# Optimization experiments

Hardware: AMD Instinct MI355X
Metric: run time of the kernel (lower is better)

## Reference

```python
import jax, jax.numpy as jnp
import numpy as np

C = 256
DEPTH = 4
GRIDS = [(128, 128), (128, 128), (128, 128)]
B = 2
N = 32768


def _ln_c(x, g, b):
    # LayerNorm over channel dim of [B, C, N] (myLayerNorm transposes to [B,N,C])
    m = x.mean(axis=1, keepdims=True)
    v = ((x - m) ** 2).mean(axis=1, keepdims=True)
    return (x - m) * jax.lax.rsqrt(v + 1e-5) * g[None, :, None] + b[None, :, None]


def _bn_train(x, g, b):
    # BatchNorm1d (training-mode batch stats) over [B, C, L]
    m = x.mean(axis=(0, 2), keepdims=True)
    v = ((x - m) ** 2).mean(axis=(0, 2), keepdims=True)
    return (x - m) * jax.lax.rsqrt(v + 1e-5) * g[None, :, None] + b[None, :, None]


def _dwconv3(x, w, b):
    # depthwise 3x3 conv, SAME padding; x [B,C,H,W], w [C,3,3]
    out = jax.lax.conv_general_dilated(x, w[:, None, :, :], (1, 1), 'SAME',
                                       feature_group_count=C,
                                       dimension_numbers=('NCHW', 'OIHW', 'NCHW'))
    return out + b[None, :, None, None]


def setup_inputs() -> dict:
    key = jax.random.key(0)
    ks = jax.random.split(key, 20)
    tokens = jax.random.normal(ks[0], (B, C, N), jnp.float32)
    hw = GRIDS[0][0] * GRIDS[0][1]
    cell_ind = jax.random.randint(ks[1], (B, 3, N), 0, hw)
    occupied_cell = jnp.ones((B, N), jnp.float32)

    def p(k, shape, scale=0.05):
        return scale * jax.random.normal(k, shape, jnp.float32)

    inp = dict(tokens=tokens, cell_ind=cell_ind, occupied_cell=occupied_cell)
    inp['smix_ln_g'] = 1.0 + p(ks[2], (DEPTH, C))
    inp['smix_ln_b'] = p(ks[3], (DEPTH, C))
    inp['ffn_w1'] = p(ks[4], (DEPTH, C, 3, 3), 0.2)
    inp['ffn_b1'] = p(ks[5], (DEPTH, C))
    inp['ffn_w2'] = p(ks[6], (DEPTH, C, 3, 3), 0.2)
    inp['ffn_b2'] = p(ks[7], (DEPTH, C))
    inp['att_scale'] = 1.0 + p(ks[8], (DEPTH, C))
    inp['att_bn_g'] = 1.0 + p(ks[9], (DEPTH, C))
    inp['att_bn_b'] = p(ks[10], (DEPTH, C))
    inp['cmix_ln_g'] = 1.0 + p(ks[11], (DEPTH, C))
    inp['cmix_ln_b'] = p(ks[12], (DEPTH, C))
    inp['cmix_w1'] = p(ks[13], (DEPTH, C, C), 1.0 / float(np.sqrt(C)))
    inp['cmix_b1'] = p(ks[14], (DEPTH, C))
    inp['cmix_w2'] = p(ks[15], (DEPTH, C, C), 1.0 / float(np.sqrt(C)))
    inp['cmix_b2'] = p(ks[16], (DEPTH, C))
    inp['cmix_scale'] = p(ks[17], (DEPTH, C), 0.1)
    return inp


def _forward(tokens, occupied_cell, cell_ind,
             smix_ln_g, smix_ln_b, ffn_w1, ffn_b1, ffn_w2, ffn_b2,
             att_scale, att_bn_g, att_bn_b,
             cmix_ln_g, cmix_ln_b, cmix_w1, cmix_b1, cmix_w2, cmix_b2, cmix_scale):
    Bx, Cx, Nx = tokens.shape
    bidx = jnp.arange(Bx)[:, None]
    # build_proj_matrix equivalent: per-point 1/(points-in-cell) weights + clamped indices
    sp = []
    for g in range(len(GRIDS)):
        HW = GRIDS[g][0] * GRIDS[g][1]
        ci = jnp.clip(cell_ind[:, g], 0, HW - 1)
        # inflate^T @ occupied: per-cell occupied count (occupied^2 per point)
        counts = jnp.zeros((Bx, HW), tokens.dtype).at[bidx, ci].add(occupied_cell * occupied_cell)
        # inflate @ counts: per-point count of points sharing its cell
        npp = occupied_cell * jnp.take_along_axis(counts, ci, axis=1)
        sp.append((ci, occupied_cell / (npp + 1e-6)))
    skip = [jnp.zeros(GRIDS[g], tokens.dtype) for g in range(len(GRIDS))]
    for d in range(DEPTH):
        g = d % len(GRIDS)
        H, W = GRIDS[g]
        HW = H * W
        ci, wpt = sp[g]
        # --- SpatialMix ---
        r = _ln_c(tokens, smix_ln_g[d], smix_ln_b[d]) * wpt[:, None, :]
        grid = jnp.zeros((Bx, Cx, HW), tokens.dtype).at[
            jnp.arange(Bx)[:, None, None], jnp.arange(Cx)[None, :, None], ci[:, None, :]].add(r)
        grid = grid.reshape(Bx, Cx, H, W) + skip[g]
        plane = _dwconv3(jax.nn.relu(_dwconv3(grid, ffn_w1[d], ffn_b1[d])), ffn_w2[d], ffn_b2[d])
        rflat = plane.reshape(Bx, Cx, HW)
        att = jax.nn.sigmoid(_bn_train(rflat * att_scale[d][None, :, None], att_bn_g[d], att_bn_b[d]))
        rflat = att * rflat
        r = jnp.take_along_axis(rflat, jnp.broadcast_to(ci[:, None, :], (Bx, Cx, Nx)), axis=2)
        tokens = tokens + r
        skip[g] = plane
        # --- ChannelMix ---
        h = _ln_c(tokens, cmix_ln_g[d], cmix_ln_b[d])
        h = jnp.einsum('oc,bcn->bon', cmix_w1[d], h) + cmix_b1[d][None, :, None]
        h = jnp.einsum('oc,bcn->bon', cmix_w2[d], jax.nn.relu(h)) + cmix_b2[d][None, :, None]
        tokens = tokens + h * cmix_scale[d][None, :, None]
    return tokens


def reference(tokens, cell_ind, occupied_cell,
              smix_ln_g, smix_ln_b, ffn_w1, ffn_b1, ffn_w2, ffn_b2,
              att_scale, att_bn_g, att_bn_b,
              cmix_ln_g, cmix_ln_b, cmix_w1, cmix_b1, cmix_w2, cmix_b2, cmix_scale):
    return _forward(tokens, occupied_cell, cell_ind,
                    smix_ln_g, smix_ln_b, ffn_w1, ffn_b1, ffn_w2, ffn_b2,
                    att_scale, att_bn_g, att_bn_b,
                    cmix_ln_g, cmix_ln_b, cmix_w1, cmix_b1, cmix_w2, cmix_b2, cmix_scale)
```

## Files before the change

### kernel.cpp

```cpp
#include <hip/hip_runtime.h>
#include <hip/hip_bf16.h>
#include <hip/hip_fp16.h>

#define Cc 256
#define Nn 32768
#define HWc 16384
#define Bb 2

typedef float floatx4 __attribute__((ext_vector_type(4)));
typedef short bf16x8 __attribute__((ext_vector_type(8)));
typedef unsigned short ushort8v __attribute__((ext_vector_type(8)));
typedef unsigned short ushort4v __attribute__((ext_vector_type(4)));

__device__ __forceinline__ unsigned short f2b(float f){
    unsigned u = __float_as_uint(f);
    u += 0x7fff + ((u >> 16) & 1);
    return (unsigned short)(u >> 16);
}
__device__ __forceinline__ float b2f(unsigned short h){
    return __uint_as_float(((unsigned)h) << 16);
}
__device__ __forceinline__ unsigned short f2h(float f){
    return __half_as_ushort(__float2half(f));
}
__device__ __forceinline__ float h2f(unsigned short h){
    return __half2float(__ushort_as_half(h));
}

__global__ __launch_bounds__(256) void k_count(const int* __restrict__ ci,
                                               const float* __restrict__ occ,
                                               float* __restrict__ fcounts,
                                               int* __restrict__ icounts){
    int idx = blockIdx.x*256 + threadIdx.x;
    if (idx >= Bb*3*Nn) return;
    int n = idx & (Nn-1);
    int bg = idx >> 15;
    int b = bg / 3;
    int cell = min(max(ci[idx], 0), HWc-1);
    float o = occ[(b<<15) + n];
    atomicAdd(&fcounts[(bg<<14) + cell], o*o);
    atomicAdd(&icounts[(bg<<14) + cell], 1);
}

__global__ __launch_bounds__(256) void k_wpt(const int* __restrict__ ci,
                                             const float* __restrict__ occ,
                                             const float* __restrict__ fcounts,
                                             float* __restrict__ wpt){
    int idx = blockIdx.x*256 + threadIdx.x;
    if (idx >= Bb*3*Nn) return;
    int n = idx & (Nn-1);
    int bg = idx >> 15;
    int b = bg / 3;
    int cell = min(max(ci[idx], 0), HWc-1);
    float o = occ[(b<<15) + n];
    float cnt = fcounts[(bg<<14) + cell];
    wpt[idx] = o / (o*cnt + 1e-6f);
}

__global__ __launch_bounds__(256) void k_scan(const int* __restrict__ ic,
                                              int* __restrict__ starts,
                                              int* __restrict__ cursor){
    __shared__ int part[256];
    int bg = blockIdx.x;
    int t = threadIdx.x;
    const int* cs = ic + (bg << 14);
    int base = t * 64;
    int s = 0;
    for (int i = 0; i < 64; ++i) s += cs[base + i];
    part[t] = s;
    __syncthreads();
    for (int off = 1; off < 256; off <<= 1){
        int v = (t >= off) ? part[t - off] : 0;
        __syncthreads();
        part[t] += v;
        __syncthreads();
    }
    int run = (t == 0) ? 0 : part[t - 1];
    int* st = starts + bg * (HWc + 1);
    int* cu = cursor + (bg << 14);
    for (int i = 0; i < 64; ++i){
        st[base + i] = run;
        cu[base + i] = run;
        run += cs[base + i];
    }
    if (t == 255) st[HWc] = run;
}

__global__ __launch_bounds__(256) void k_fill(const int* __restrict__ ci,
                                              int* __restrict__ cursor,
                                              int* __restrict__ plist){
    int idx = blockIdx.x*256 + threadIdx.x;
    if (idx >= Bb*3*Nn) return;
    int n = idx & (Nn-1);
    int bg = idx >> 15;
    int cell = min(max(ci[idx], 0), HWc-1);
    int pos = atomicAdd(&cursor[(bg<<14) + cell], 1);
    plist[(bg<<15) + pos] = n;
}

__global__ __launch_bounds__(256) void k_wcvt(const float* __restrict__ w1,
                                              const float* __restrict__ w2,
                                              unsigned short* __restrict__ W1b,
                                              unsigned short* __restrict__ W2b){
    int idx = blockIdx.x*256 + threadIdx.x;
    if (idx >= 4*Cc*Cc) return;
    W1b[idx] = f2b(w1[idx]);
    W2b[idx] = f2b(w2[idx]);
}

__global__ __launch_bounds__(512, 4) void k1a_ln(const float* __restrict__ tok,
                                              const float* __restrict__ wpt,
                                              const float* __restrict__ lng,
                                              const float* __restrict__ lnb,
                                              unsigned short* __restrict__ rbuf, int g){
    __shared__ float reds[512], redq[512];
    __shared__ float m_s[64], r_s[64];
    __shared__ float lg[Cc], lb[Cc];
    int tid = threadIdx.x;
    int bi = blockIdx.x;
    int b = bi >> 9;
    int p0 = (bi & 511) << 6;
    if (tid < 256){ lg[tid] = lng[tid]; lb[tid] = lnb[tid]; }
    int p  = tid & 63;
    int cg = tid >> 6;
    int c0 = cg << 5;
    const float* tb = tok + ((size_t)b << 8)*Nn + p0 + p;
    float vreg[32];
    float sum = 0.f, sq = 0.f;
    #pragma unroll
    for (int k = 0; k < 32; ++k){
        float v = tb[(size_t)(c0 + k) << 15];
        vreg[k] = v; sum += v; sq += v*v;
    }
    reds[tid] = sum; redq[tid] = sq;
    __syncthreads();
    if (tid < 64){
        float s = 0.f, q = 0.f;
        #pragma unroll
        for (int j = 0; j < 8; ++j){ s += reds[j*64 + tid]; q += redq[j*64 + tid]; }
        float m = s * (1.f/256.f);
        float var = q * (1.f/256.f) - m*m;
        m_s[tid] = m;
        r_s[tid] = rsqrtf(fmaxf(var, 0.f) + 1e-5f);
    }
    __syncthreads();
    float mp = m_s[p], rp = r_s[p];
    float wv = wpt[(b*3 + g)*Nn + p0 + p];
    unsigned short* rb = rbuf + ((size_t)((b << 15) + p0 + p))*Cc + c0;
    #pragma unroll
    for (int j = 0; j < 4; ++j){
        ushort8v u;
        #pragma unroll
        for (int e = 0; e < 8; ++e){
            int k = j*8 + e, c = c0 + k;
            u[e] = f2h(((vreg[k] - mp)*rp*lg[c] + lb[c]) * wv);
        }
        *(ushort8v*)(rb + 8*j) = u;
    }
}

__global__ __launch_bounds__(256) void k1b_gather(const unsigned short* __restrict__ rbuf,
                                                  const int* __restrict__ starts,
                                                  const int* __restrict__ plist,
                                                  unsigned short* __restrict__ grid,
                                                  float* __restrict__ bnSQ, int g){
    int t = threadIdx.x;
    int bi = blockIdx.x;
    if (bi == 0){ bnSQ[t] = 0.f; bnSQ[256 + t] = 0.f; }
    int b = bi >> 11;
    int cell0 = (bi & 2047) << 3;
    int bg = b*3 + g;
    const int* st = starts + bg*(HWc + 1) + cell0;
    const int* pl = plist + (bg << 15);
    const unsigned short* rb = rbuf + (((size_t)b << 15) << 8);
    float acc[8];
    int s0 = st[0];
    #pragma unroll
    for (int q = 0; q < 8; ++q){
        int s1 = st[q + 1];
        float a = 0.f;
        for (int j = s0; j < s1; ++j){
            int p = pl[j];
            a += h2f(rb[((size_t)p << 8) + t]);
        }
        acc[q] = a;
        s0 = s1;
    }
    unsigned short* go = grid + ((size_t)((b << 8) + t))*HWc + cell0;
    ushort8v u;
    #pragma unroll
    for (int e = 0; e < 8; ++e) u[e] = f2h(acc[e]);
    *(ushort8v*)go = u;
}

__global__ __launch_bounds__(256) void k2_conv(const unsigned short* __restrict__ grid,
                                               const unsigned short* __restrict__ skip,
                                               unsigned short* __restrict__ plane,
                                               const float* __restrict__ w1, const float* __restrict__ b1,
                                               const float* __restrict__ w2, const float* __restrict__ b2,
                                               const float* __restrict__ asc,
                                               float* __restrict__ bnS, float* __restrict__ bnQ,
                                               int useskip){
    __shared__ float it[36*136];
    __shared__ float mid[34*136];
    int tid = threadIdx.x;
    int bi = blockIdx.x;
    int rt = bi & 3;
    int bc = bi >> 2;
    int c = bc & 255;
    int r0 = rt << 5;
    const unsigned short* src = grid + (size_t)bc*HWc;
    const unsigned short* sk  = skip + (size_t)bc*HWc;
    for (int i = tid; i < 36; i += 256){
        it[i*136 + 0] = 0.f;   it[i*136 + 1] = 0.f;
        it[i*136 + 130] = 0.f; it[i*136 + 131] = 0.f;
        it[i*136 + 132] = 0.f; it[i*136 + 133] = 0.f;
    }
    for (int i = tid; i < 36*16; i += 256){
        int r = i >> 4, ch = i & 15;
        int gy = r0 - 2 + r;
        float vals[8];
        #pragma unroll
        for (int e = 0; e < 8; ++e) vals[e] = 0.f;
        if ((unsigned)gy < 128u){
            ushort8v sv = *(const ushort8v*)(src + (gy << 7) + ch*8);
            if (useskip){
                ushort8v kv = *(const ushort8v*)(sk + (gy << 7) + ch*8);
                #pragma unroll
                for (int e = 0; e < 8; ++e) vals[e] = h2f(sv[e]) + h2f(kv[e]);
            } else {
                #pragma unroll
                for (int e = 0; e < 8; ++e) vals[e] = h2f(sv[e]);
            }
        }
        #pragma unroll
        for (int e = 0; e < 8; ++e) it[r*136 + 2 + ch*8 + e] = vals[e];
    }
    float a1[9], a2[9];
    #pragma unroll
    for (int j = 0; j < 9; ++j){ a1[j] = w1[c*9+j]; a2[j] = w2[c*9+j]; }
    float bb1 = b1[c], bb2 = b2[c], sc = asc[c];
    __syncthreads();
    for (int i = tid; i < 34*33; i += 256){
        int r = i / 33, chk = i - r*33;
        int cc0 = chk << 2;
        int y = r0 - 1 + r;
        bool yok = (unsigned)y < 128u;
        float o0 = 0.f, o1 = 0.f, o2 = 0.f, o3 = 0.f;
        if (yok){
            #pragma unroll
            for (int jr = 0; jr < 3; ++jr){
                const float* row = &it[(r + jr)*136 + cc0];
                floatx4 a = *(const floatx4*)row;
                float a4 = row[4], a5 = row[5];
                float w0 = a1[jr*3+0], w1v = a1[jr*3+1], w2v = a1[jr*3+2];
                o0 += w0*a[0] + w1v*a[1] + w2v*a[2];
                o1 += w0*a[1] + w1v*a[2] + w2v*a[3];
                o2 += w0*a[2] + w1v*a[3] + w2v*a4;
                o3 += w0*a[3] + w1v*a4  + w2v*a5;
            }
        }
        float* mrow = &mid[r*136 + cc0];
        mrow[0] = (yok && cc0+0 >= 1 && cc0+0 <= 128) ? fmaxf(o0 + bb1, 0.f) : 0.f;
        mrow[1] = (yok && cc0+1 >= 1 && cc0+1 <= 128) ? fmaxf(o1 + bb1, 0.f) : 0.f;
        mrow[2] = (yok && cc0+2 >= 1 && cc0+2 <= 128) ? fmaxf(o2 + bb1, 0.f) : 0.f;
        mrow[3] = (yok && cc0+3 >= 1 && cc0+3 <= 128) ? fmaxf(o3 + bb1, 0.f) : 0.f;
    }
    __syncthreads();
    float ps = 0.f, pq = 0.f;
    unsigned short* dst = plane + (size_t)bc*HWc;
    for (int i = tid; i < 32*32; i += 256){
        int yy = i >> 5, chk = i & 31;
        int x0 = chk << 2;
        float o0 = 0.f, o1 = 0.f, o2 = 0.f, o3 = 0.f;
        #pragma unroll
        for (int jr = 0; jr < 3; ++jr){
            const float* row = &mid[(yy + jr)*136 + x0];
            floatx4 a = *(const floatx4*)row;
            float a4 = row[4], a5 = row[5];
            float w0 = a2[jr*3+0], w1v = a2[jr*3+1], w2v = a2[jr*3+2];
            o0 += w0*a[0] + w1v*a[1] + w2v*a[2];
            o1 += w0*a[1] + w1v*a[2] + w2v*a[3];
            o2 += w0*a[2] + w1v*a[3] + w2v*a4;
            o3 += w0*a[3] + w1v*a4  + w2v*a5;
        }
        float v0 = o0 + bb2, v1 = o1 + bb2, v2 = o2 + bb2, v3 = o3 + bb2;
        ushort4v u;
        u[0] = f2h(v0); u[1] = f2h(v1); u[2] = f2h(v2); u[3] = f2h(v3);
        *(ushort4v*)(dst + ((r0 + yy) << 7) + x0) = u;
        float t0 = v0*sc, t1 = v1*sc, t2 = v2*sc, t3 = v3*sc;
        ps += t0 + t1 + t2 + t3;
        pq += t0*t0 + t1*t1 + t2*t2 + t3*t3;
    }
    __syncthreads();
    it[tid] = ps; it[256 + tid] = pq;
    __syncthreads();
    for (int s2 = 128; s2 > 0; s2 >>= 1){
        if (tid < s2){ it[tid] += it[tid+s2]; it[256+tid] += it[256+tid+s2]; }
        __syncthreads();
    }
    if (tid == 0){
        atomicAdd(&bnS[c], it[0]);
        atomicAdd(&bnQ[c], it[256]);
    }
}

__global__ __launch_bounds__(256) void k3t_att_t(const unsigned short* __restrict__ plane,
                                                 const float* __restrict__ bnS, const float* __restrict__ bnQ,
                                                 const float* __restrict__ asc,
                                                 const float* __restrict__ bng, const float* __restrict__ bnb,
                                                 unsigned short* __restrict__ attp){
    __shared__ float t[32*33];
    __shared__ float P_s[32], Q_s[32];
    int tid = threadIdx.x;
    int tx = tid & 31, ty = tid >> 5;
    int bi = blockIdx.x;
    int ht = bi & 511;
    int ct = (bi >> 9) & 7;
    int b  = bi >> 12;
    int c0 = ct << 5, h0 = ht << 5;
    if (tid < 32){
        int c = c0 + tid;
        float mean = bnS[c] * (1.f/32768.f);
        float var  = bnQ[c] * (1.f/32768.f) - mean*mean;
        float inv  = rsqrtf(fmaxf(var, 0.f) + 1e-5f) * bng[c];
        P_s[tid] = asc[c] * inv;
        Q_s[tid] = bnb[c] - mean * inv;
    }
    __syncthreads();
    for (int r = ty; r < 32; r += 8){
        int c = c0 + r;
        float v = h2f(plane[(((size_t)b << 8) + c)*HWc + h0 + tx]);
        float s = 1.f / (1.f + __expf(-(P_s[r]*v + Q_s[r])));
        t[r*33 + tx] = s * v;
    }
    __syncthreads();
    for (int r = ty; r < 32; r += 8){
        attp[(((size_t)b << 14) + h0 + r)*Cc + c0 + tx] = f2h(t[tx*33 + r]);
    }
}

__global__ __launch_bounds__(512, 4) void k4_cmix(const float* __restrict__ tsrc, int tin_nc,
                                               float* __restrict__ tdst, int tout_nc,
                                               const unsigned short* __restrict__ attp,
                                               const int* __restrict__ ci,
                                               const unsigned short* __restrict__ W1,
                                               const unsigned short* __restrict__ W2,
                                               const float* __restrict__ lng, const float* __restrict__ lnb,
                                               const float* __restrict__ b1, const float* __restrict__ b2,
                                               const float* __restrict__ csc,
                                               const float* __restrict__ lng2, const float* __restrict__ lnb2,
                                               const float* __restrict__ wptb,
                                               unsigned short* __restrict__ rbufn,
                                               int g, int g2, int donext){
    __shared__ __align__(16) unsigned short hs[64*264];
    __shared__ float reds[512], redq[512];
    __shared__ float m_s[64], r_s[64];
    __shared__ int cell_s[64];
    __shared__ float lng_s[Cc], lnb_s[Cc], b1_s[Cc], b2s_s[Cc], cs_s[Cc], g2g_s[Cc], g2b_s[Cc];

    int tid = threadIdx.x;
    int bi = blockIdx.x;
    int b = bi >> 9;
    int p0 = (bi & 511) << 6;

    if (tid < 256){
        lng_s[tid] = lng[tid];
        lnb_s[tid] = lnb[tid];
        b1_s[tid]  = b1[tid];
        float cv = csc[tid];
        cs_s[tid]  = cv;
        b2s_s[tid] = b2[tid] * cv;
        g2g_s[tid] = lng2[tid];
        g2b_s[tid] = lnb2[tid];
    }
    if (tid < 64){
        int cc = ci[(b*3 + g)*Nn + p0 + tid];
        cell_s[tid] = min(max(cc, 0), HWc-1);
    }
    __syncthreads();

    int p  = tid & 63;
    int cg = tid >> 6;
    int c0 = cg << 5;

    const unsigned short* ar = attp + ((size_t)((b << 14) + cell_s[p]))*Cc + c0;
    ushort8v rr[4];
    #pragma unroll
    for (int j = 0; j < 4; ++j) rr[j] = *(const ushort8v*)(ar + 8*j);

    float vreg[32];
    float sum = 0.f, sq = 0.f;
    if (tin_nc){
        const floatx4* tn4 = (const floatx4*)(tsrc + ((((size_t)(b << 15)) + p0 + p) << 8) + c0);
        #pragma unroll
        for (int j = 0; j < 8; ++j){
            floatx4 f = tn4[j];
            #pragma unroll
            for (int e = 0; e < 4; ++e){
                int k = j*4 + e;
                float v = f[e] + h2f(rr[k >> 3][k & 7]);
                vreg[k] = v; sum += v; sq += v*v;
            }
        }
    } else {
        const float* tb = tsrc + ((size_t)b << 8)*Nn + p0 + p;
        #pragma unroll
        for (int k = 0; k < 32; ++k){
            float v = tb[(size_t)(c0 + k) << 15] + h2f(rr[k >> 3][k & 7]);
            vreg[k] = v; sum += v; sq += v*v;
        }
    }
    reds[tid] = sum; redq[tid] = sq;
    __syncthreads();
    if (tid < 64){
        float s = 0.f, q = 0.f;
        #pragma unroll
        for (int j = 0; j < 8; ++j){ s += reds[j*64 + tid]; q += redq[j*64 + tid]; }
        float m = s * (1.f/256.f);
        float var = q * (1.f/256.f) - m*m;
        m_s[tid] = m;
        r_s[tid] = rsqrtf(fmaxf(var, 0.f) + 1e-5f);
    }
    __syncthreads();
    float mp = m_s[p], rp = r_s[p];
    unsigned short* hrow = &hs[p*264 + c0];
    #pragma unroll
    for (int j = 0; j < 4; ++j){
        ushort8v u;
        #pragma unroll
        for (int e = 0; e < 8; ++e){
            int k = j*8 + e, c = c0 + k;
            u[e] = f2b((vreg[k] - mp)*rp*lng_s[c] + lnb_s[c]);
        }
        *(ushort8v*)(hrow + 8*j) = u;
    }
    __syncthreads();

    int lane = tid & 63;
    int w = tid >> 6;
    int l15 = lane & 15;
    int q4 = lane >> 4;
    floatx4 acc[2][4];
    #pragma unroll
    for (int mi = 0; mi < 2; ++mi)
        #pragma unroll
        for (int ni = 0; ni < 4; ++ni)
            acc[mi][ni] = (floatx4){0.f, 0.f, 0.f, 0.f};

    #pragma unroll
    for (int kk = 0; kk < 8; ++kk){
        int k0 = kk*32 + q4*8;
        bf16x8 bfr[4];
        #pragma unroll
        for (int ni = 0; ni < 4; ++ni)
            bfr[ni] = *(const bf16x8*)&hs[(ni*16 + l15)*264 + k0];
        #pragma unroll
        for (int mi = 0; mi < 2; ++mi){
            bf16x8 af = *(const bf16x8*)&W1[(size_t)(w*32 + mi*16 + l15)*Cc + k0];
            #pragma unroll
            for (int ni = 0; ni < 4; ++ni)
                acc[mi][ni] = __builtin_amdgcn_mfma_f32_16x16x32_bf16(af, bfr[ni], acc[mi][ni], 0, 0, 0);
        }
    }
    __syncthreads();
    #pragma unroll
    for (int mi = 0; mi < 2; ++mi)
        #pragma unroll
        for (int ni = 0; ni < 4; ++ni){
            int m0 = w*32 + mi*16 + q4*4;
            int nn = ni*16 + l15;
            ushort4v u;
            #pragma unroll
            for (int r = 0; r < 4; ++r)
                u[r] = f2b(fmaxf(acc[mi][ni][r] + b1_s[m0 + r], 0.f));
            *(ushort4v*)&hs[nn*264 + m0] = u;
        }
    __syncthreads();

    #pragma unroll
    for (int mi = 0; mi < 2; ++mi)
        #pragma unroll
        for (int ni = 0; ni < 4; ++ni)
            acc[mi][ni] = (floatx4){0.f, 0.f, 0.f, 0.f};
    #pragma unroll
    for (int kk = 0; kk < 8; ++kk){
        int k0 = kk*32 + q4*8;
        bf16x8 bfr[4];
        #pragma unroll
        for (int ni = 0; ni < 4; ++ni)
            bfr[ni] = *(const bf16x8*)&hs[(ni*16 + l15)*264 + k0];
        #pragma unroll
        for (int mi = 0; mi < 2; ++mi){
            bf16x8 af = *(const bf16x8*)&W2[(size_t)(w*32 + mi*16 + l15)*Cc + k0];
            #pragma unroll
            for (int ni = 0; ni < 4; ++ni)
                acc[mi][ni] = __builtin_amdgcn_mfma_f32_16x16x32_bf16(af, bfr[ni], acc[mi][ni], 0, 0, 0);
        }
    }
    __syncthreads();
    #pragma unroll
    for (int mi = 0; mi < 2; ++mi)
        #pragma unroll
        for (int ni = 0; ni < 4; ++ni){
            int m0 = w*32 + mi*16 + q4*4;
            int nn = ni*16 + l15;
            ushort4v u;
            #pragma unroll
            for (int r = 0; r < 4; ++r)
                u[r] = f2b(acc[mi][ni][r]*cs_s[m0 + r] + b2s_s[m0 + r]);
            *(ushort4v*)&hs[nn*264 + m0] = u;
        }
    __syncthreads();

    float sum2 = 0.f, sq2 = 0.f;
    if (tout_nc){
        float* tn = tdst + ((((size_t)(b << 15)) + p0 + p) << 8) + c0;
        #pragma unroll
        for (int j = 0; j < 4; ++j){
            ushort8v u = *(const ushort8v*)(hrow + 8*j);
            floatx4 fa, fb;
            #pragma unroll
            for (int e = 0; e < 4; ++e){
                int k = j*8 + e;
                float v = vreg[k] + b2f(u[e]);
                vreg[k] = v; fa[e] = v; sum2 += v; sq2 += v*v;
            }
            #pragma unroll
            for (int e = 4; e < 8; ++e){
                int k = j*8 + e;
                float v = vreg[k] + b2f(u[e]);
                vreg[k] = v; fb[e-4] = v; sum2 += v; sq2 += v*v;
            }
            *(floatx4*)(tn + 8*j) = fa;
            *(floatx4*)(tn + 8*j + 4) = fb;
        }
    } else {
        float* ob = tdst + ((size_t)b << 8)*Nn + p0 + p;
        #pragma unroll
        for (int j = 0; j < 4; ++j){
            ushort8v u = *(const ushort8v*)(hrow + 8*j);
            #pragma unroll
            for (int e = 0; e < 8; ++e){
                int k = j*8 + e, c = c0 + k;
                float v = vreg[k] + b2f(u[e]);
                vreg[k] = v;
                ob[(size_t)c << 15] = v;
                sum2 += v; sq2 += v*v;
            }
        }
    }
    if (donext){
        reds[tid] = sum2; redq[tid] = sq2;
        __syncthreads();
        if (tid < 64){
            float s = 0.f, q = 0.f;
            #pragma unroll
            for (int j = 0; j < 8; ++j){ s += reds[j*64 + tid]; q += redq[j*64 + tid]; }
            float m = s * (1.f/256.f);
            float var = q * (1.f/256.f) - m*m;
            m_s[tid] = m;
            r_s[tid] = rsqrtf(fmaxf(var, 0.f) + 1e-5f);
        }
        __syncthreads();
        float m2 = m_s[p], rr2 = r_s[p];
        float wv2 = wptb[(b*3 + g2)*Nn + p0 + p];
        unsigned short* rb = rbufn + ((size_t)((b << 15) + p0 + p))*Cc + c0;
        #pragma unroll
        for (int j = 0; j < 4; ++j){
            ushort8v u;
            #pragma unroll
            for (int e = 0; e < 8; ++e){
                int k = j*8 + e, c = c0 + k;
                u[e] = f2h(((vreg[k] - m2)*rr2*g2g_s[c] + g2b_s[c]) * wv2);
            }
            *(ushort8v*)(rb + 8*j) = u;
        }
    }
}

extern "C" void kernel_launch(void* const* d_in, const int* in_sizes, int n_in,
                              void* d_out, int out_size, void* d_ws, size_t ws_size,
                              hipStream_t stream){
    (void)in_sizes; (void)n_in; (void)out_size;
    const float* tokens  = (const float*)d_in[0];
    const int*   cellind = (const int*)d_in[1];
    const float* occ     = (const float*)d_in[2];
    const float* smix_g  = (const float*)d_in[3];
    const float* smix_b  = (const float*)d_in[4];
    const float* ffn_w1  = (const float*)d_in[5];
    const float* ffn_b1  = (const float*)d_in[6];
    const float* ffn_w2  = (const float*)d_in[7];
    const float* ffn_b2  = (const float*)d_in[8];
    const float* att_sc  = (const float*)d_in[9];
    const float* bn_g    = (const float*)d_in[10];
    const float* bn_b    = (const float*)d_in[11];
    const float* cm_g    = (const float*)d_in[12];
    const float* cm_b    = (const float*)d_in[13];
    const float* cw1     = (const float*)d_in[14];
    const float* cb1     = (const float*)d_in[15];
    const float* cw2     = (const float*)d_in[16];
    const float* cb2     = (const float*)d_in[17];
    const float* cscale  = (const float*)d_in[18];
    float* out = (float*)d_out;
    char* w = (char*)d_ws;

    const size_t HGRID_BYTES = (size_t)Bb*Cc*HWc*2;
    unsigned short* grid_h  = (unsigned short*)(w);
    unsigned short* attp_h  = grid_h;
    unsigned short* planeA  = (unsigned short*)(w + HGRID_BYTES);
    unsigned short* planeB  = (unsigned short*)(w + 2*HGRID_BYTES);
    unsigned short* rbuf    = (unsigned short*)(w + 3*HGRID_BYTES);
    size_t o = 3*HGRID_BYTES + (size_t)Bb*Nn*Cc*2;
    float* fcounts = (float*)(w + o); o += (size_t)Bb*3*HWc*4;
    int*   icounts = (int*)(w + o);   o += (size_t)Bb*3*HWc*4;
    float* wptb   = (float*)(w + o); o += (size_t)Bb*3*Nn*4;
    float* bnS    = (float*)(w + o);
    float* bnQ    = bnS + 256;
    o += 4096;
    unsigned short* W1b = (unsigned short*)(w + o);
    unsigned short* W2b = W1b + 4*Cc*Cc;
    o += (size_t)2*4*Cc*Cc*2;
    int* startsb  = (int*)(w + o); o += (size_t)Bb*3*(HWc+1)*4;
    int* cursors  = (int*)(w + o); o += (size_t)Bb*3*HWc*4;
    int* plistb   = (int*)(w + o); o += (size_t)Bb*3*Nn*4;
    o = (o + 255) & ~(size_t)255;
    float* tnc    = (float*)(w + o);
    size_t needed = o + (size_t)Bb*Nn*Cc*4;
    int nc_ok = (ws_size >= needed) ? 1 : 0;

    hipMemsetAsync(fcounts, 0, (size_t)2*Bb*3*HWc*4, stream);
    k_count<<<(Bb*3*Nn)/256, 256, 0, stream>>>(cellind, occ, fcounts, icounts);
    k_wpt<<<(Bb*3*Nn)/256, 256, 0, stream>>>(cellind, occ, fcounts, wptb);
    k_scan<<<Bb*3, 256, 0, stream>>>(icounts, startsb, cursors);
    k_fill<<<(Bb*3*Nn)/256, 256, 0, stream>>>(cellind, cursors, plistb);
    k_wcvt<<<(4*Cc*Cc)/256, 256, 0, stream>>>(cw1, cw2, W1b, W2b);

    k1a_ln<<<Bb*(Nn/64), 512, 0, stream>>>(tokens, wptb, smix_g, smix_b, rbuf, 0);

    for (int d = 0; d < 4; ++d){
        int g = d % 3;
        int g2 = (d + 1) % 3;
        int donext = (d < 3) ? 1 : 0;
        int useskip = (d == 3) ? 1 : 0;
        unsigned short* plane = (d == 0) ? planeA : planeB;
        int dn = (d + 1 < 4) ? d + 1 : d;

        const float* tsrc; int tin_nc;
        float* tdst; int tout_nc;
        if (nc_ok){
            tsrc = (d == 0) ? tokens : tnc;  tin_nc  = (d == 0) ? 0 : 1;
            tdst = (d == 3) ? out : tnc;     tout_nc = (d == 3) ? 0 : 1;
        } else {
            tsrc = (d == 0) ? tokens : out;  tin_nc  = 0;
            tdst = out;                      tout_nc = 0;
        }

        k1b_gather<<<Bb*(HWc/8), 256, 0, stream>>>(rbuf, startsb, plistb, grid_h, bnS, g);
        k2_conv<<<Bb*Cc*4, 256, 0, stream>>>(grid_h, planeA, plane,
                                             ffn_w1 + d*Cc*9, ffn_b1 + d*Cc,
                                             ffn_w2 + d*Cc*9, ffn_b2 + d*Cc,
                                             att_sc + d*Cc, bnS, bnQ, useskip);
        k3t_att_t<<<Bb*8*512, 256, 0, stream>>>(plane, bnS, bnQ, att_sc + d*Cc,
                                                bn_g + d*Cc, bn_b + d*Cc, attp_h);
        k4_cmix<<<Bb*(Nn/64), 512, 0, stream>>>(tsrc, tin_nc, tdst, tout_nc, attp_h, cellind,
                                                W1b + (size_t)d*Cc*Cc, W2b + (size_t)d*Cc*Cc,
                                                cm_g + d*Cc, cm_b + d*Cc,
                                                cb1 + d*Cc, cb2 + d*Cc, cscale + d*Cc,
                                                smix_g + dn*Cc, smix_b + dn*Cc, wptb,
                                                rbuf, g, g2, donext);
    }
}
```

Baseline: 702.9 us.

## Add specialized token-major channel-mix kernel for middle depths and fuse setup kernels

Adds k4_cmix_nc, a version of the channel-mix kernel for depths 1-2 that reads and writes tokens in [B,N,C] layout. It keeps the hidden activations in LDS, runs both 256x256 projections with bf16 MFMA, and produces the next layer's normalized, weighted rbuf in one pass. The setup path folds the weight-per-token kernel into the fill kernel, vectorizes the scan with int4 loads and stores, and pads the starts stride to keep those accesses aligned. The aim is fewer launches and less generic indexing on the middle layers, at the cost of a second code path to keep correct.

```diff
diff --git a/kernel.cpp b/kernel.cpp
--- a/kernel.cpp
+++ b/kernel.cpp
@@ -6,11 +6,13 @@
 #define Nn 32768
 #define HWc 16384
 #define Bb 2
+#define STS (HWc + 16)
 
 typedef float floatx4 __attribute__((ext_vector_type(4)));
 typedef short bf16x8 __attribute__((ext_vector_type(8)));
 typedef unsigned short ushort8v __attribute__((ext_vector_type(8)));
 typedef unsigned short ushort4v __attribute__((ext_vector_type(4)));
+typedef int int4v __attribute__((ext_vector_type(4)));
 
 __device__ __forceinline__ unsigned short f2b(float f){
     unsigned u = __float_as_uint(f);
@@ -42,10 +44,48 @@
     atomicAdd(&icounts[(bg<<14) + cell], 1);
 }
 
-__global__ __launch_bounds__(256) void k_wpt(const int* __restrict__ ci,
-                                             const float* __restrict__ occ,
-                                             const float* __restrict__ fcounts,
-                                             float* __restrict__ wpt){
+__global__ __launch_bounds__(256) void k_scan(const int* __restrict__ ic,
+                                              int* __restrict__ starts,
+                                              int* __restrict__ cursor){
+    __shared__ int part[256];
+    int bg = blockIdx.x;
+    int t = threadIdx.x;
+    const int* cs = ic + (bg << 14);
+    int4v buf[16];
+    int s = 0;
+    #pragma unroll
+    for (int i = 0; i < 16; ++i){
+        buf[i] = *(const int4v*)(cs + t*64 + i*4);
+        s += buf[i][0] + buf[i][1] + buf[i][2] + buf[i][3];
+    }
+    part[t] = s;
+    __syncthreads();
+    for (int off = 1; off < 256; off <<= 1){
+        int v = (t >= off) ? part[t - off] : 0;
+        __syncthreads();
+        part[t] += v;
+        __syncthreads();
+    }
+    int run = (t == 0) ? 0 : part[t - 1];
+    int* st = starts + bg * STS;
+    int* cu = cursor + (bg << 14);
+    #pragma unroll
+    for (int i = 0; i < 16; ++i){
+        int4v o;
+        #pragma unroll
+        for (int e = 0; e < 4; ++e){ o[e] = run; run += buf[i][e]; }
+        *(int4v*)(st + t*64 + i*4) = o;
+        *(int4v*)(cu + t*64 + i*4) = o;
+    }
+    if (t == 255) st[HWc] = run;
+}
+
+__global__ __launch_bounds__(256) void k_fill(const int* __restrict__ ci,
+                                              const float* __restrict__ occ,
+                                              const float* __restrict__ fcounts,
+                                              int* __restrict__ cursor,
+                                              int* __restrict__ plist,
+                                              float* __restrict__ wpt){
     int idx = blockIdx.x*256 + threadIdx.x;
     if (idx >= Bb*3*Nn) return;
     int n = idx & (Nn-1);
@@ -55,45 +95,6 @@
     float o = occ[(b<<15) + n];
     float cnt = fcounts[(bg<<14) + cell];
     wpt[idx] = o / (o*cnt + 1e-6f);
-}
-
-__global__ __launch_bounds__(256) void k_scan(const int* __restrict__ ic,
-                                              int* __restrict__ starts,
-                                              int* __restrict__ cursor){
-    __shared__ int part[256];
-    int bg = blockIdx.x;
-    int t = threadIdx.x;
-    const int* cs = ic + (bg << 14);
-    int base = t * 64;
-    int s = 0;
-    for (int i = 0; i < 64; ++i) s += cs[base + i];
-    part[t] = s;
-    __syncthreads();
-    for (int off = 1; off < 256; off <<= 1){
-        int v = (t >= off) ? part[t - off] : 0;
-        __syncthreads();
-        part[t] += v;
-        __syncthreads();
-    }
-    int run = (t == 0) ? 0 : part[t - 1];
-    int* st = starts + bg * (HWc + 1);
-    int* cu = cursor + (bg << 14);
-    for (int i = 0; i < 64; ++i){
-        st[base + i] = run;
-        cu[base + i] = run;
-        run += cs[base + i];
-    }
-    if (t == 255) st[HWc] = run;
-}
-
-__global__ __launch_bounds__(256) void k_fill(const int* __restrict__ ci,
-                                              int* __restrict__ cursor,
-                                              int* __restrict__ plist){
-    int idx = blockIdx.x*256 + threadIdx.x;
-    if (idx >= Bb*3*Nn) return;
-    int n = idx & (Nn-1);
-    int bg = idx >> 15;
-    int cell = min(max(ci[idx], 0), HWc-1);
     int pos = atomicAdd(&cursor[(bg<<14) + cell], 1);
     plist[(bg<<15) + pos] = n;
 }
@@ -170,7 +171,7 @@
     int b = bi >> 11;
     int cell0 = (bi & 2047) << 3;
     int bg = b*3 + g;
-    const int* st = starts + bg*(HWc + 1) + cell0;
+    const int* st = starts + bg*STS + cell0;
     const int* pl = plist + (bg << 15);
     const unsigned short* rb = rbuf + (((size_t)b << 15) << 8);
     float acc[8];
@@ -576,6 +577,184 @@
             }
             *(ushort8v*)(rb + 8*j) = u;
         }
+    }
+}
+
+__global__ __launch_bounds__(512, 4) void k4_cmix_nc(const float* __restrict__ tsrc,
+                                               float* __restrict__ tdst,
+                                               const unsigned short* __restrict__ attp,
+                                               const int* __restrict__ ci,
+                                               const unsigned short* __restrict__ W1,
+                                               const unsigned short* __restrict__ W2,
+                                               const float* __restrict__ lng, const float* __restrict__ lnb,
+                                               const float* __restrict__ b1, const float* __restrict__ b2,
+                                               const float* __restrict__ csc,
+                                               const float* __restrict__ lng2, const float* __restrict__ lnb2,
+                                               const float* __restrict__ wptb,
+                                               unsigned short* __restrict__ rbufn,
+                                               int g, int g2){
+    __shared__ __align__(16) unsigned short hs[64*264];
+    __shared__ float b1_s[Cc], b2s_s[Cc], cs_s[Cc];
+
+    int tid = threadIdx.x;
+    int lane = tid & 63;
+    int w = tid >> 6;
+    int bi = blockIdx.x;
+    int b = bi >> 9;
+    int p0 = (bi & 511) << 6;
+    int c4 = lane << 2;
+
+    if (tid < 256){
+        b1_s[tid]  = b1[tid];
+        float cv = csc[tid];
+        cs_s[tid]  = cv;
+        b2s_s[tid] = b2[tid] * cv;
+    }
+
+    floatx4 lngv = *(const floatx4*)&lng[c4];
+    floatx4 lnbv = *(const floatx4*)&lnb[c4];
+
+    int cells[8];
+    const int pb = (b*3 + g)*Nn + p0 + w*8;
+    #pragma unroll
+    for (int i = 0; i < 8; ++i){
+        int cc = ci[pb + i];
+        cells[i] = min(max(cc, 0), HWc-1);
+    }
+
+    #pragma unroll
+    for (int i = 0; i < 8; ++i){
+        int p = w*8 + i;
+        ushort4v av = *(const ushort4v*)(attp + ((size_t)((b << 14) + cells[i]))*Cc + c4);
+        floatx4 tv = *(const floatx4*)(tsrc + ((size_t)((b << 15) + p0 + p))*Cc + c4);
+        floatx4 v4;
+        float s = 0.f, q = 0.f;
+        #pragma unroll
+        for (int e = 0; e < 4; ++e){
+            float v = tv[e] + h2f(av[e]);
+            v4[e] = v; s += v; q += v*v;
+        }
+        #pragma unroll
+        for (int m = 1; m < 64; m <<= 1){
+            s += __shfl_xor(s, m, 64);
+            q += __shfl_xor(q, m, 64);
+        }
+        float mean = s * (1.f/256.f);
+        float var  = q * (1.f/256.f) - mean*mean;
+        float rinv = rsqrtf(fmaxf(var, 0.f) + 1e-5f);
+        ushort4v u;
+        #pragma unroll
+        for (int e = 0; e < 4; ++e)
+            u[e] = f2b((v4[e] - mean)*rinv*lngv[e] + lnbv[e]);
+        *(ushort4v*)&hs[p*264 + c4] = u;
+    }
+    __syncthreads();
+
+    int l15 = lane & 15;
+    int q4 = lane >> 4;
+    floatx4 acc[2][4];
+    #pragma unroll
+    for (int mi = 0; mi < 2; ++mi)
+        #pragma unroll
+        for (int ni = 0; ni < 4; ++ni)
+            acc[mi][ni] = (floatx4){0.f, 0.f, 0.f, 0.f};
+
+    #pragma unroll
+    for (int kk = 0; kk < 8; ++kk){
+        int k0 = kk*32 + q4*8;
+        bf16x8 bfr[4];
+        #pragma unroll
+        for (int ni = 0; ni < 4; ++ni)
+            bfr[ni] = *(const bf16x8*)&hs[(ni*16 + l15)*264 + k0];
+        #pragma unroll
+        for (int mi = 0; mi < 2; ++mi){
+            bf16x8 af = *(const bf16x8*)&W1[(size_t)(w*32 + mi*16 + l15)*Cc + k0];
+            #pragma unroll
+            for (int ni = 0; ni < 4; ++ni)
+                acc[mi][ni] = __builtin_amdgcn_mfma_f32_16x16x32_bf16(af, bfr[ni], acc[mi][ni], 0, 0, 0);
+        }
+    }
+    __syncthreads();
+    #pragma unroll
+    for (int mi = 0; mi < 2; ++mi)
+        #pragma unroll
+        for (int ni = 0; ni < 4; ++ni){
+            int m0 = w*32 + mi*16 + q4*4;
+            int nn = ni*16 + l15;
+            ushort4v u;
+            #pragma unroll
+            for (int r = 0; r < 4; ++r)
+                u[r] = f2b(fmaxf(acc[mi][ni][r] + b1_s[m0 + r], 0.f));
+            *(ushort4v*)&hs[nn*264 + m0] = u;
+        }
+    __syncthreads();
+
+    #pragma unroll
+    for (int mi = 0; mi < 2; ++mi)
+        #pragma unroll
+        for (int ni = 0; ni < 4; ++ni)
+            acc[mi][ni] = (floatx4){0.f, 0.f, 0.f, 0.f};
+    #pragma unroll
+    for (int kk = 0; kk < 8; ++kk){
+        int k0 = kk*32 + q4*8;
+        bf16x8 bfr[4];
+        #pragma unroll
+        for (int ni = 0; ni < 4; ++ni)
+            bfr[ni] = *(const bf16x8*)&hs[(ni*16 + l15)*264 + k0];
+        #pragma unroll
+        for (int mi = 0; mi < 2; ++mi){
+            bf16x8 af = *(const bf16x8*)&W2[(size_t)(w*32 + mi*16 + l15)*Cc + k0];
+            #pragma unroll
+            for (int ni = 0; ni < 4; ++ni)
+                acc[mi][ni] = __builtin_amdgcn_mfma_f32_16x16x32_bf16(af, bfr[ni], acc[mi][ni], 0, 0, 0);
+        }
+    }
+    __syncthreads();
+    #pragma unroll
+    for (int mi = 0; mi < 2; ++mi)
+        #pragma unroll
+        for (int ni = 0; ni < 4; ++ni){
+            int m0 = w*32 + mi*16 + q4*4;
+            int nn = ni*16 + l15;
+            ushort4v u;
+            #pragma unroll
+            for (int r = 0; r < 4; ++r)
+                u[r] = f2b(acc[mi][ni][r]*cs_s[m0 + r] + b2s_s[m0 + r]);
+            *(ushort4v*)&hs[nn*264 + m0] = u;
+        }
+    __syncthreads();
+
+    floatx4 g2gv = *(const floatx4*)&lng2[c4];
+    floatx4 g2bv = *(const floatx4*)&lnb2[c4];
+    const int pb2 = (b*3 + g2)*Nn + p0 + w*8;
+    #pragma unroll
+    for (int i = 0; i < 8; ++i){
+        int p = w*8 + i;
+        ushort4v av = *(const ushort4v*)(attp + ((size_t)((b << 14) + cells[i]))*Cc + c4);
+        floatx4 tv = *(const floatx4*)(tsrc + ((size_t)((b << 15) + p0 + p))*Cc + c4);
+        ushort4v hv = *(const ushort4v*)&hs[p*264 + c4];
+        floatx4 v4;
+        float s = 0.f, q = 0.f;
+        #pragma unroll
+        for (int e = 0; e < 4; ++e){
+            float v = tv[e] + h2f(av[e]) + b2f(hv[e]);
+            v4[e] = v; s += v; q += v*v;
+        }
+        *(floatx4*)(tdst + ((size_t)((b << 15) + p0 + p))*Cc + c4) = v4;
+        #pragma unroll
+        for (int m = 1; m < 64; m <<= 1){
+            s += __shfl_xor(s, m, 64);
+            q += __shfl_xor(q, m, 64);
+        }
+        float mean = s * (1.f/256.f);
+        float var  = q * (1.f/256.f) - mean*mean;
+        float rinv = rsqrtf(fmaxf(var, 0.f) + 1e-5f);
+        float wv = wptb[pb2 + i];
+        ushort4v u;
+        #pragma unroll
+        for (int e = 0; e < 4; ++e)
+            u[e] = f2h(((v4[e] - mean)*rinv*g2gv[e] + g2bv[e]) * wv);
+        *(ushort4v*)(rbufn + ((size_t)((b << 15) + p0 + p))*Cc + c4) = u;
     }
 }
 
@@ -621,7 +800,7 @@
     unsigned short* W1b = (unsigned short*)(w + o);
     unsigned short* W2b = W1b + 4*Cc*Cc;
     o += (size_t)2*4*Cc*Cc*2;
-    int* startsb  = (int*)(w + o); o += (size_t)Bb*3*(HWc+1)*4;
+    int* startsb  = (int*)(w + o); o += (size_t)Bb*3*STS*4;
     int* cursors  = (int*)(w + o); o += (size_t)Bb*3*HWc*4;
     int* plistb   = (int*)(w + o); o += (size_t)Bb*3*Nn*4;
     o = (o + 255) & ~(size_t)255;
@@ -631,9 +810,8 @@
 
     hipMemsetAsync(fcounts, 0, (size_t)2*Bb*3*HWc*4, stream);
     k_count<<<(Bb*3*Nn)/256, 256, 0, stream>>>(cellind, occ, fcounts, icounts);
-    k_wpt<<<(Bb*3*Nn)/256, 256, 0, stream>>>(cellind, occ, fcounts, wptb);
     k_scan<<<Bb*3, 256, 0, stream>>>(icounts, startsb, cursors);
-    k_fill<<<(Bb*3*Nn)/256, 256, 0, stream>>>(cellind, cursors, plistb);
+    k_fill<<<(Bb*3*Nn)/256, 256, 0, stream>>>(cellind, occ, fcounts, cursors, plistb, wptb);
     k_wcvt<<<(4*Cc*Cc)/256, 256, 0, stream>>>(cw1, cw2, W1b, W2b);
 
     k1a_ln<<<Bb*(Nn/64), 512, 0, stream>>>(tokens, wptb, smix_g, smix_b, rbuf, 0);
@@ -663,11 +841,20 @@
                                              att_sc + d*Cc, bnS, bnQ, useskip);
         k3t_att_t<<<Bb*8*512, 256, 0, stream>>>(plane, bnS, bnQ, att_sc + d*Cc,
                                                 bn_g + d*Cc, bn_b + d*Cc, attp_h);
-        k4_cmix<<<Bb*(Nn/64), 512, 0, stream>>>(tsrc, tin_nc, tdst, tout_nc, attp_h, cellind,
+        if (nc_ok && d >= 1 && d <= 2){
+            k4_cmix_nc<<<Bb*(Nn/64), 512, 0, stream>>>(tnc, tnc, attp_h, cellind,
+                                                W1b + (size_t)d*Cc*Cc, W2b + (size_t)d*Cc*Cc,
+                                                cm_g + d*Cc, cm_b + d*Cc,
+                                                cb1 + d*Cc, cb2 + d*Cc, cscale + d*Cc,
+                                                smix_g + dn*Cc, smix_b + dn*Cc, wptb,
+                                                rbuf, g, g2);
+        } else {
+            k4_cmix<<<Bb*(Nn/64), 512, 0, stream>>>(tsrc, tin_nc, tdst, tout_nc, attp_h, cellind,
                                                 W1b + (size_t)d*Cc*Cc, W2b + (size_t)d*Cc*Cc,
                                                 cm_g + d*Cc, cm_b + d*Cc,
                                                 cb1 + d*Cc, cb2 + d*Cc, cscale + d*Cc,
                                                 smix_g + dn*Cc, smix_b + dn*Cc, wptb,
                                                 rbuf, g, g2, donext);
-    }
-}
+        }
+    }
+}
```

After: 690.0 us. About the same (-1.8%).
